# Kernel optimization log

Hardware: AMD Instinct MI355X
Metric: run time of the kernel (lower is better)

The kernel has to match this reference:

```python
import jax, jax.numpy as jnp
import numpy as np

B, S, D, H = 8, 1024, 1024, 16
DH = D // H
LN_EPS = 1e-5
SLOPE = 0.01  # nn.LeakyReLU default negative_slope


def _ln(x, g, b):
    m = x.mean(-1, keepdims=True)
    v = ((x - m) ** 2).mean(-1, keepdims=True)
    return (x - m) / jnp.sqrt(v + LN_EPS) * g + b


def _leaky(x):
    return jnp.where(x >= 0, x, SLOPE * x)


def setup_inputs() -> dict:
    key = jax.random.key(0)
    ks = jax.random.split(key, 6)
    q = jax.random.normal(ks[0], (B, S, D), dtype=jnp.float32)
    masks = jnp.ones((B, S), dtype=jnp.int32)  # all-valid mask (masked_fill is a no-op)
    w1 = jax.random.normal(ks[1], (D, D), dtype=jnp.float32) * 0.02
    b1 = jnp.zeros((D,), jnp.float32)
    w2 = jax.random.normal(ks[2], (D, D), dtype=jnp.float32) * 0.02
    b2 = jnp.zeros((D,), jnp.float32)
    ones = jnp.ones((D,), jnp.float32)
    zeros = jnp.zeros((D,), jnp.float32)
    return dict(q=q, masks=masks,
                w1=w1, b1=b1, ln1_g=ones, ln1_b=zeros,
                w2=w2, b2=b2, ln2_g=ones, ln2_b=zeros,
                anf_g=ones, anf_b=zeros,
                an1_g=ones, an1_b=zeros,
                an2_g=ones, an2_b=zeros)


def reference(q, masks, w1, b1, ln1_g, ln1_b, w2, b2, ln2_g, ln2_b,
              anf_g, anf_b, an1_g, an1_b, an2_g, an2_b):
    # --- multi-head cosine-similarity attention (k = v = q, no projections) ---
    qh = q.reshape(B, S, H, DH).transpose(0, 2, 1, 3)  # (B,H,S,DH) == separate_heads
    qn = qh / jnp.clip(jnp.linalg.norm(qh, axis=-1, keepdims=True), 1e-8)
    # cosine similarity scores, softmax over keys
    w = jax.nn.softmax(jnp.einsum('bhqd,bhkd->bhqk', qn, qn), axis=-1)
    # masked_fill AFTER softmax (faithful to source: mask per (batch, query))
    w = jnp.where(masks[:, None, :, None] == 0, jnp.float32(-1e9), w)
    heads = jnp.einsum('bhqk,bhkd->bhqd', w, qh)
    attn = heads.transpose(0, 2, 1, 3).reshape(B, S, D)  # concat_heads
    # --- add_norm1 (dropout=0.5 but eval mode => identity) ---
    y1 = _ln(q + attn, an1_g, an1_b)
    # --- PositionWiseFFN: Linear->LN->LeakyReLU x2, then internal AddNorm ---
    h = _leaky(_ln(y1 @ w1 + b1, ln1_g, ln1_b))
    y = _leaky(_ln(h @ w2 + b2, ln2_g, ln2_b))
    y2 = _ln(y1 + y, anf_g, anf_b)
    # --- add_norm2 ---
    return _ln(y1 + y2, an2_g, an2_b)
```

## Files before the change

kernel.cpp:

```cpp
#include <hip/hip_runtime.h>
#include <hip/hip_bf16.h>

#define BB 8
#define SS 1024
#define DD 1024
#define HH 16

typedef __attribute__((ext_vector_type(8))) short short8;
typedef __attribute__((ext_vector_type(8))) __bf16 bf16x8;
typedef __attribute__((ext_vector_type(4))) float f32x4;

__device__ inline float bf2f(unsigned short h){
  unsigned u = ((unsigned)h) << 16;
  return __builtin_bit_cast(float, u);
}
__device__ inline unsigned short f2bf(float f){
  unsigned u = __builtin_bit_cast(unsigned, f);
  u += 0x7fffu + ((u >> 16) & 1u);
  return (unsigned short)(u >> 16);
}
__device__ inline f32x4 mfma16(short8 a, short8 b, f32x4 c){
  return __builtin_amdgcn_mfma_f32_16x16x32_bf16(
      __builtin_bit_cast(bf16x8, a), __builtin_bit_cast(bf16x8, b), c, 0, 0, 0);
}
__device__ inline void gld_lds16(const unsigned short* g, unsigned short* l){
  __builtin_amdgcn_global_load_lds((const __attribute__((address_space(1))) void*)g,
      (__attribute__((address_space(3))) void*)l, 16, 0, 0);
}

__global__ __launch_bounds__(256) void prep_w(const float* __restrict__ w1,
                                              const float* __restrict__ w2,
                                              unsigned short* __restrict__ w1T,
                                              unsigned short* __restrict__ w2T){
  __shared__ float tile[64][65];
  const float* src = blockIdx.z ? w2 : w1;
  unsigned short* dst = blockIdx.z ? w2T : w1T;
  int k0 = blockIdx.x * 64, n0 = blockIdx.y * 64;
  int tx = threadIdx.x & 63, ty = threadIdx.x >> 6;
#pragma unroll
  for (int r = 0; r < 16; ++r)
    tile[ty + 4*r][tx] = src[(k0 + ty + 4*r) * DD + n0 + tx];
  __syncthreads();
#pragma unroll
  for (int r = 0; r < 16; ++r)
    dst[(n0 + ty + 4*r) * DD + k0 + tx] = f2bf(tile[tx][ty + 4*r]);
}

__global__ __launch_bounds__(256) void prep_q(const float* __restrict__ q,
                                              unsigned short* __restrict__ kf,
                                              unsigned short* __restrict__ vf,
                                              unsigned short* __restrict__ qb){
  __shared__ float tile[64][65];
  __shared__ float rinv[64];
  int bh = blockIdx.x >> 4, st = blockIdx.x & 15;
  int b = bh >> 4, h = bh & 15;
  int t = threadIdx.x;
  int tx = t & 63, ty = t >> 6;
  int srow = b * SS + st * 64;
#pragma unroll
  for (int r = 0; r < 16; ++r)
    tile[ty + 4*r][tx] = q[(size_t)(srow + ty + 4*r) * DD + h * 64 + tx];
  __syncthreads();
  {
    int s = t >> 2, p = t & 3;
    float ssum = 0.f;
#pragma unroll
    for (int i = 0; i < 16; ++i){ float v = tile[s][p*16 + i]; ssum += v * v; }
    ssum += __shfl_xor(ssum, 1);
    ssum += __shfl_xor(ssum, 2);
    if (p == 0) rinv[s] = 1.0f / fmaxf(sqrtf(ssum), 1e-8f);
  }
  __syncthreads();
#pragma unroll
  for (int r = 0; r < 16; ++r)
    qb[(size_t)(srow + ty + 4*r) * DD + h * 64 + tx] = f2bf(tile[ty + 4*r][tx]);
#pragma unroll
  for (int v = 0; v < 2; ++v){
    int idx = t * 2 + v;
    int c_l = idx >> 6, lane = idx & 63;
    int g2 = c_l >> 2, c = (c_l >> 1) & 1, hf = c_l & 1;
    int lrq = lane & 15, lgq = lane >> 4;
    int s = g2 * 32 + (lrq >> 2) * 8 + c * 4 + (lrq & 3);
    int d0 = hf * 32 + lgq * 8;
    float rv = rinv[s] * 1.20112240878645f;
    short8 o;
#pragma unroll
    for (int e = 0; e < 8; ++e) o[e] = (short)f2bf(tile[s][d0 + e] * rv);
    *(short8*)(kf + ((size_t)(bh * 128 + st * 8 + c_l) * 64 + lane) * 8) = o;
  }
#pragma unroll
  for (int v = 0; v < 2; ++v){
    int idx = t * 2 + v;
    int kt2 = idx >> 8, db = (idx >> 6) & 3, lane = idx & 63;
    int d = db * 16 + (lane & 15);
    int k0 = kt2 * 32 + (lane >> 4) * 8;
    short8 o;
#pragma unroll
    for (int e = 0; e < 8; ++e) o[e] = (short)f2bf(tile[k0 + e][d]);
    *(short8*)(vf + ((size_t)((bh * 32 + st * 2 + kt2) * 4 + db) * 512 + lane * 8)) = o;
  }
}

#define NPH 16
__global__ __launch_bounds__(512, 4) void attn_kern(const unsigned short* __restrict__ kf,
                                                    const unsigned short* __restrict__ vf,
                                                    const int* __restrict__ masks,
                                                    unsigned short* __restrict__ attnb){
  __shared__ unsigned short Kb[3][8][512];
  __shared__ unsigned short Vb[3][8][512];
  __shared__ int anym;
  const int bh = blockIdx.x, b = bh >> 4, h = bh & 15;
  const int by = blockIdx.y;
  const int t = threadIdx.x, w = t >> 6, l = t & 63;
  const int lr = l & 15, lg = l >> 4;
  if (t == 0) anym = 0;
  __syncthreads();
  if (t < 256 && masks[b * SS + by * 256 + t] == 0) anym = 1;

  short8 aQ[2][2];
#pragma unroll
  for (int c = 0; c < 2; ++c)
#pragma unroll
    for (int hf = 0; hf < 2; ++hf)
      aQ[c][hf] = *(const short8*)(kf +
          ((size_t)(bh * 128 + (by * 8 + w) * 4 + c * 2 + hf) * 64 + l) * 8);

  const short ONEB = (short)0x3F80;
  const short8 ones = {ONEB, ONEB, ONEB, ONEB, ONEB, ONEB, ONEB, ONEB};

#define STAGE(ph, bf) do {                                                            \
    if (w < 4){                                                                       \
      gld_lds16(kf + ((size_t)(bh * 128 + (2*(ph)) * 4 + w) * 64 + l) * 8,            \
                &Kb[bf][w][0]);                                                       \
      gld_lds16(kf + ((size_t)(bh * 128 + (2*(ph)+1) * 4 + w) * 64 + l) * 8,          \
                &Kb[bf][4 + w][0]);                                                   \
    } else {                                                                          \
      gld_lds16(vf + ((size_t)((bh * 32 + 2*(ph)) * 4 + (w - 4)) * 512 + l * 8),      \
                &Vb[bf][w - 4][0]);                                                   \
      gld_lds16(vf + ((size_t)((bh * 32 + 2*(ph)+1) * 4 + (w - 4)) * 512 + l * 8),    \
                &Vb[bf][4 + (w - 4)][0]);                                             \
    }                                                                                 \
  } while (0)

  STAGE(0, 0);
  STAGE(1, 1);
  asm volatile("s_waitcnt vmcnt(2) lgkmcnt(0)" ::: "memory");
  __builtin_amdgcn_s_barrier();

  f32x4 o[2][4] = {};
  f32x4 rsacc[2] = {};

  for (int ph = 0; ph < NPH; ++ph){
    const int cur = ph % 3;
    if (ph + 2 < NPH) STAGE(ph + 2, (ph + 2) % 3);
#pragma unroll
    for (int gi = 0; gi < 2; ++gi){
      short8 bK[2][2];
#pragma unroll
      for (int c = 0; c < 2; ++c)
#pragma unroll
        for (int hf = 0; hf < 2; ++hf)
          bK[c][hf] = *(const short8*)&Kb[cur][gi * 4 + c * 2 + hf][l * 8];
      f32x4 sc[2][2];
#pragma unroll
      for (int qc = 0; qc < 2; ++qc)
#pragma unroll
        for (int c = 0; c < 2; ++c){
          f32x4 z = {0.f, 0.f, 0.f, 0.f};
          z = mfma16(bK[c][0], aQ[qc][0], z);
          z = mfma16(bK[c][1], aQ[qc][1], z);
          sc[qc][c] = z;
        }
      bf16x8 pav[2];
#pragma unroll
      for (int qc = 0; qc < 2; ++qc)
#pragma unroll
        for (int c = 0; c < 2; ++c)
#pragma unroll
          for (int j = 0; j < 4; ++j){
            float x = sc[qc][c][j], pv;
            asm("v_exp_f32 %0, %1" : "=v"(pv) : "v"(x));
            pav[qc][c * 4 + j] = (__bf16)pv;
          }
      short8 pa0 = __builtin_bit_cast(short8, pav[0]);
      short8 pa1 = __builtin_bit_cast(short8, pav[1]);
      rsacc[0] = mfma16(pa0, ones, rsacc[0]);
      rsacc[1] = mfma16(pa1, ones, rsacc[1]);
#pragma unroll
      for (int db = 0; db < 4; ++db){
        short8 bV = *(const short8*)&Vb[cur][gi * 4 + db][l * 8];
        o[0][db] = mfma16(pa0, bV, o[0][db]);
        o[1][db] = mfma16(pa1, bV, o[1][db]);
      }
    }
    if (ph + 1 < NPH){
      asm volatile("s_waitcnt lgkmcnt(0)" ::: "memory");
      if (ph + 2 < NPH) asm volatile("s_waitcnt vmcnt(2)" ::: "memory");
      else              asm volatile("s_waitcnt vmcnt(0)" ::: "memory");
      __builtin_amdgcn_s_barrier();
    }
  }

#pragma unroll
  for (int qc = 0; qc < 2; ++qc){
    float invj[4];
#pragma unroll
    for (int j = 0; j < 4; ++j) invj[j] = 1.0f / rsacc[qc][j];
#pragma unroll
    for (int db = 0; db < 4; ++db)
#pragma unroll
      for (int j = 0; j < 4; ++j){
        int qrow = by * 256 + w * 32 + lg * 8 + qc * 4 + j;
        float val = o[qc][db][j] * invj[j];
        if (anym && masks[b * SS + qrow] == 0){
          float vs = 0.f;
          for (int kt = 0; kt < 32; ++kt)
            for (int lgp = 0; lgp < 4; ++lgp){
              const unsigned short* vp = vf +
                  ((size_t)((bh * 32 + kt) * 4 + db) * 512 + (lgp * 16 + lr) * 8);
              for (int e = 0; e < 8; ++e) vs += bf2f(vp[e]);
            }
          val = -1e9f * vs;
        }
        attnb[(size_t)(b * SS + qrow) * DD + h * 64 + db * 16 + lr] = f2bf(val);
      }
  }
#undef STAGE
}

__device__ inline float2 br2(float a, float bq){
  __shared__ float sm[8];
#pragma unroll
  for (int off = 1; off < 64; off <<= 1){
    a += __shfl_xor(a, off);
    bq += __shfl_xor(bq, off);
  }
  int w = threadIdx.x >> 6;
  if ((threadIdx.x & 63) == 0){ sm[w * 2] = a; sm[w * 2 + 1] = bq; }
  __syncthreads();
  int base = (threadIdx.x >> 7) * 4;
  float2 r;
  r.x = sm[base] + sm[base + 2];
  r.y = sm[base + 1] + sm[base + 3];
  __syncthreads();
  return r;
}

__global__ __launch_bounds__(256) void addnorm1(const unsigned short* __restrict__ qb,
                                                const unsigned short* __restrict__ attnb,
                                                const float* __restrict__ g,
                                                const float* __restrict__ bt,
                                                unsigned short* __restrict__ y1b){
  int rg = threadIdx.x >> 7, tt = threadIdx.x & 127;
  int row = blockIdx.x * 2 + rg;
  short8 qv = *(const short8*)(qb + (size_t)row * DD + tt * 8);
  short8 av = *(const short8*)(attnb + (size_t)row * DD + tt * 8);
  float x[8]; float s = 0.f, ssq = 0.f;
#pragma unroll
  for (int i = 0; i < 8; ++i){
    x[i] = bf2f((unsigned short)qv[i]) + bf2f((unsigned short)av[i]);
    s += x[i]; ssq += x[i] * x[i];
  }
  float2 r = br2(s, ssq);
  float m = r.x * (1.0f / DD);
  float rs = rsqrtf(r.y * (1.0f / DD) - m * m + 1e-5f);
  float4 g0 = *(const float4*)(g + tt * 8), g1 = *(const float4*)(g + tt * 8 + 4);
  float4 b0 = *(const float4*)(bt + tt * 8), b1 = *(const float4*)(bt + tt * 8 + 4);
  float gg[8] = {g0.x,g0.y,g0.z,g0.w,g1.x,g1.y,g1.z,g1.w};
  float bb[8] = {b0.x,b0.y,b0.z,b0.w,b1.x,b1.y,b1.z,b1.w};
  short8 ob;
#pragma unroll
  for (int i = 0; i < 8; ++i) ob[i] = (short)f2bf((x[i]-m)*rs*gg[i] + bb[i]);
  *(short8*)(y1b + (size_t)row * DD + tt * 8) = ob;
}

__global__ __launch_bounds__(256, 2) void gemm_bias(const unsigned short* __restrict__ X,
                                                    const unsigned short* __restrict__ WT,
                                                    const float* __restrict__ bias,
                                                    unsigned short* __restrict__ out){
  __shared__ unsigned short LDSB[24576];
  int t = threadIdx.x, l = t & 63, w = t >> 6;
  int wm = w >> 1, wn = w & 1;
  int lr = l & 15, lg = l >> 4;
  int bm = blockIdx.x * 128, bn = blockIdx.y * 128;
  f32x4 acc[4][4] = {};
  int r = t >> 2, cb = (t & 3) * 8;

#define ASP(bf) (LDSB + (bf) * 4096)
#define BSP(bf) (LDSB + 12288 + (bf) * 4096)
#define GSTAGE(kt, bf) do {                                                        \
    gld_lds16(X  + (size_t)(bm +      r) * 1024 + (kt) * 32 + cb,                  \
              ASP(bf) + w * 512);                                                  \
    gld_lds16(X  + (size_t)(bm + 64 + r) * 1024 + (kt) * 32 + cb,                  \
              ASP(bf) + 2048 + w * 512);                                           \
    gld_lds16(WT + (size_t)(bn +      r) * 1024 + (kt) * 32 + cb,                  \
              BSP(bf) + w * 512);                                                  \
    gld_lds16(WT + (size_t)(bn + 64 + r) * 1024 + (kt) * 32 + cb,                  \
              BSP(bf) + 2048 + w * 512);                                           \
  } while (0)

  GSTAGE(0, 0);
  GSTAGE(1, 1);
  asm volatile("s_waitcnt vmcnt(4)" ::: "memory");
  __builtin_amdgcn_s_barrier();

  for (int kt = 0; kt < 32; ++kt){
    const int cur = kt % 3;
    if (kt + 2 < 32) GSTAGE(kt + 2, (kt + 2) % 3);
    short8 aA[4], bB[4];
#pragma unroll
    for (int i = 0; i < 4; ++i)
      aA[i] = *(const short8*)(ASP(cur) + (wm * 64 + i * 16 + lr) * 32 + lg * 8);
#pragma unroll
    for (int i = 0; i < 4; ++i)
      bB[i] = *(const short8*)(BSP(cur) + (wn * 64 + i * 16 + lr) * 32 + lg * 8);
    __builtin_amdgcn_s_setprio(1);
#pragma unroll
    for (int mi = 0; mi < 4; ++mi)
#pragma unroll
      for (int ni = 0; ni < 4; ++ni)
        acc[mi][ni] = mfma16(aA[mi], bB[ni], acc[mi][ni]);
    __builtin_amdgcn_s_setprio(0);
    if (kt + 1 < 32){
      asm volatile("s_waitcnt lgkmcnt(0)" ::: "memory");
      if (kt + 2 < 32) asm volatile("s_waitcnt vmcnt(4)" ::: "memory");
      else             asm volatile("s_waitcnt vmcnt(0)" ::: "memory");
      __builtin_amdgcn_s_barrier();
    }
  }
#undef GSTAGE

  asm volatile("s_waitcnt lgkmcnt(0)" ::: "memory");
  __builtin_amdgcn_s_barrier();
#pragma unroll
  for (int ni = 0; ni < 4; ++ni){
    int col = wn * 64 + ni * 16 + lr;
    float bv = bias[bn + col];
#pragma unroll
    for (int mi = 0; mi < 4; ++mi){
      int row0 = wm * 64 + mi * 16 + lg * 4;
#pragma unroll
      for (int j = 0; j < 4; ++j)
        LDSB[(row0 + j) * 128 + col] = f2bf(acc[mi][ni][j] + bv);
    }
  }
  asm volatile("s_waitcnt lgkmcnt(0)" ::: "memory");
  __builtin_amdgcn_s_barrier();
#pragma unroll
  for (int i = 0; i < 8; ++i){
    int idx = t + i * 256;
    int row = idx >> 4;
    int c8  = idx & 15;
    short8 v = *(const short8*)&LDSB[row * 128 + c8 * 8];
    *(short8*)(out + (size_t)(bm + row) * 1024 + bn + c8 * 8) = v;
  }
#undef ASP
#undef BSP
}

__global__ __launch_bounds__(256) void ln_leaky(const unsigned short* __restrict__ in,
                                                const float* __restrict__ g,
                                                const float* __restrict__ bt,
                                                unsigned short* __restrict__ out){
  int rg = threadIdx.x >> 7, tt = threadIdx.x & 127;
  int row = blockIdx.x * 2 + rg;
  short8 iv = *(const short8*)(in + (size_t)row * DD + tt * 8);
  float x[8]; float s = 0.f, ssq = 0.f;
#pragma unroll
  for (int i = 0; i < 8; ++i){
    x[i] = bf2f((unsigned short)iv[i]);
    s += x[i]; ssq += x[i] * x[i];
  }
  float2 r = br2(s, ssq);
  float m = r.x * (1.0f / DD);
  float rs = rsqrtf(r.y * (1.0f / DD) - m * m + 1e-5f);
  float4 g0 = *(const float4*)(g + tt * 8), g1 = *(const float4*)(g + tt * 8 + 4);
  float4 b0 = *(const float4*)(bt + tt * 8), b1 = *(const float4*)(bt + tt * 8 + 4);
  float gg[8] = {g0.x,g0.y,g0.z,g0.w,g1.x,g1.y,g1.z,g1.w};
  float bb[8] = {b0.x,b0.y,b0.z,b0.w,b1.x,b1.y,b1.z,b1.w};
  short8 ov;
#pragma unroll
  for (int i = 0; i < 8; ++i){
    float v = (x[i]-m)*rs*gg[i] + bb[i];
    v = v >= 0.f ? v : 0.01f * v;
    ov[i] = (short)f2bf(v);
  }
  *(short8*)(out + (size_t)row * DD + tt * 8) = ov;
}

__global__ __launch_bounds__(256) void final_kern(const unsigned short* __restrict__ g2,
                                                  const unsigned short* __restrict__ y1,
                                                  const float* __restrict__ ln2g, const float* __restrict__ ln2b,
                                                  const float* __restrict__ anfg, const float* __restrict__ anfb,
                                                  const float* __restrict__ an2g, const float* __restrict__ an2b,
                                                  float* __restrict__ out){
  int rg = threadIdx.x >> 7, tt = threadIdx.x & 127;
  int row = blockIdx.x * 2 + rg;
  short8 iv = *(const short8*)(g2 + (size_t)row * DD + tt * 8);
  short8 yv = *(const short8*)(y1 + (size_t)row * DD + tt * 8);
  float x[8], yy1[8]; float s = 0.f, ssq = 0.f;
#pragma unroll
  for (int i = 0; i < 8; ++i){
    x[i] = bf2f((unsigned short)iv[i]);
    yy1[i] = bf2f((unsigned short)yv[i]);
    s += x[i]; ssq += x[i] * x[i];
  }
  float2 r = br2(s, ssq);
  float m = r.x * (1.0f / DD);
  float rs = rsqrtf(r.y * (1.0f / DD) - m * m + 1e-5f);
  float4 p0, p1;
  p0 = *(const float4*)(ln2g + tt * 8); p1 = *(const float4*)(ln2g + tt * 8 + 4);
  float gg[8] = {p0.x,p0.y,p0.z,p0.w,p1.x,p1.y,p1.z,p1.w};
  p0 = *(const float4*)(ln2b + tt * 8); p1 = *(const float4*)(ln2b + tt * 8 + 4);
  float bb[8] = {p0.x,p0.y,p0.z,p0.w,p1.x,p1.y,p1.z,p1.w};
  float y[8];
#pragma unroll
  for (int i = 0; i < 8; ++i){
    float v = (x[i]-m)*rs*gg[i] + bb[i];
    y[i] = v >= 0.f ? v : 0.01f * v;
  }

  float tv[8]; s = 0.f; ssq = 0.f;
#pragma unroll
  for (int i = 0; i < 8; ++i){ tv[i] = yy1[i] + y[i]; s += tv[i]; ssq += tv[i]*tv[i]; }
  r = br2(s, ssq);
  m = r.x * (1.0f / DD);
  rs = rsqrtf(r.y * (1.0f / DD) - m*m + 1e-5f);
  p0 = *(const float4*)(anfg + tt * 8); p1 = *(const float4*)(anfg + tt * 8 + 4);
  float gg2[8] = {p0.x,p0.y,p0.z,p0.w,p1.x,p1.y,p1.z,p1.w};
  p0 = *(const float4*)(anfb + tt * 8); p1 = *(const float4*)(anfb + tt * 8 + 4);
  float bb2[8] = {p0.x,p0.y,p0.z,p0.w,p1.x,p1.y,p1.z,p1.w};
  float y2[8];
#pragma unroll
  for (int i = 0; i < 8; ++i) y2[i] = (tv[i]-m)*rs*gg2[i] + bb2[i];

  float u[8]; s = 0.f; ssq = 0.f;
#pragma unroll
  for (int i = 0; i < 8; ++i){ u[i] = yy1[i] + y2[i]; s += u[i]; ssq += u[i]*u[i]; }
  r = br2(s, ssq);
  m = r.x * (1.0f / DD);
  rs = rsqrtf(r.y * (1.0f / DD) - m*m + 1e-5f);
  p0 = *(const float4*)(an2g + tt * 8); p1 = *(const float4*)(an2g + tt * 8 + 4);
  float gg3[8] = {p0.x,p0.y,p0.z,p0.w,p1.x,p1.y,p1.z,p1.w};
  p0 = *(const float4*)(an2b + tt * 8); p1 = *(const float4*)(an2b + tt * 8 + 4);
  float bb3[8] = {p0.x,p0.y,p0.z,p0.w,p1.x,p1.y,p1.z,p1.w};
  float4 o0 = { (u[0]-m)*rs*gg3[0] + bb3[0], (u[1]-m)*rs*gg3[1] + bb3[1],
                (u[2]-m)*rs*gg3[2] + bb3[2], (u[3]-m)*rs*gg3[3] + bb3[3] };
  float4 o1 = { (u[4]-m)*rs*gg3[4] + bb3[4], (u[5]-m)*rs*gg3[5] + bb3[5],
                (u[6]-m)*rs*gg3[6] + bb3[6], (u[7]-m)*rs*gg3[7] + bb3[7] };
  *(float4*)(out + (size_t)row * DD + tt * 8) = o0;
  *(float4*)(out + (size_t)row * DD + tt * 8 + 4) = o1;
}

extern "C" void kernel_launch(void* const* d_in, const int* in_sizes, int n_in,
                              void* d_out, int out_size, void* d_ws, size_t ws_size,
                              hipStream_t stream){
  const float* q    = (const float*)d_in[0];
  const int* masks  = (const int*)d_in[1];
  const float* w1   = (const float*)d_in[2];
  const float* b1   = (const float*)d_in[3];
  const float* ln1g = (const float*)d_in[4];
  const float* ln1b = (const float*)d_in[5];
  const float* w2   = (const float*)d_in[6];
  const float* b2   = (const float*)d_in[7];
  const float* ln2g = (const float*)d_in[8];
  const float* ln2b = (const float*)d_in[9];
  const float* anfg = (const float*)d_in[10];
  const float* anfb = (const float*)d_in[11];
  const float* an1g = (const float*)d_in[12];
  const float* an1b = (const float*)d_in[13];
  const float* an2g = (const float*)d_in[14];
  const float* an2b = (const float*)d_in[15];

  char* ws = (char*)d_ws;
  unsigned short* w1T  = (unsigned short*)(ws + 0);
  unsigned short* w2T  = (unsigned short*)(ws + 2097152);
  unsigned short* kf   = (unsigned short*)(ws + 4194304);
  unsigned short* vf   = (unsigned short*)(ws + 20971520);
  unsigned short* attn = (unsigned short*)(ws + 37748736);
  unsigned short* y1b  = (unsigned short*)(ws + 54525952);
  unsigned short* qb   = (unsigned short*)(ws + 71303168);
  unsigned short* g1   = kf;
  unsigned short* hbuf = vf;
  unsigned short* g2   = attn;
  float* outp = (float*)d_out;

  prep_w<<<dim3(16, 16, 2), 256, 0, stream>>>(w1, w2, w1T, w2T);
  prep_q<<<dim3(2048), 256, 0, stream>>>(q, kf, vf, qb);
  attn_kern<<<dim3(128, 4), 512, 0, stream>>>(kf, vf, masks, attn);
  addnorm1<<<dim3(4096), 256, 0, stream>>>(qb, attn, an1g, an1b, y1b);
  gemm_bias<<<dim3(64, 8), 256, 0, stream>>>(y1b, w1T, b1, g1);
  ln_leaky<<<dim3(4096), 256, 0, stream>>>(g1, ln1g, ln1b, hbuf);
  gemm_bias<<<dim3(64, 8), 256, 0, stream>>>(hbuf, w2T, b2, g2);
  final_kern<<<dim3(4096), 256, 0, stream>>>(g2, y1b, ln2g, ln2b, anfg, anfb, an2g, an2b, outp);
}
```

Baseline: 144.1 us.

## Halve attention block to 4 waves, each computing 64 query rows

The attention kernel now runs 256 threads per block instead of 512. Each wave handles four 16-row query chunks instead of two, so every K/V fragment read from LDS feeds twice as many MFMAs. Staging is redistributed so each of the four waves issues four global-to-LDS loads per phase, and the vmcnt waits are adjusted to match. This cuts LDS read traffic and barrier participants per unit of work. In exchange it raises register pressure (larger accumulators, launch bounds lowered) and gives fewer waves per CU to hide latency.

Result: no change. 142.5 us (-1.2%).

```diff
diff --git a/kernel.cpp b/kernel.cpp
--- a/kernel.cpp
+++ b/kernel.cpp
@@ -102,7 +102,7 @@
 }
 
 #define NPH 16
-__global__ __launch_bounds__(512, 4) void attn_kern(const unsigned short* __restrict__ kf,
+__global__ __launch_bounds__(256, 2) void attn_kern(const unsigned short* __restrict__ kf,
                                                     const unsigned short* __restrict__ vf,
                                                     const int* __restrict__ masks,
                                                     unsigned short* __restrict__ attnb){
@@ -115,40 +115,40 @@
   const int lr = l & 15, lg = l >> 4;
   if (t == 0) anym = 0;
   __syncthreads();
-  if (t < 256 && masks[b * SS + by * 256 + t] == 0) anym = 1;
-
-  short8 aQ[2][2];
-#pragma unroll
-  for (int c = 0; c < 2; ++c)
+  if (masks[b * SS + by * 256 + t] == 0) anym = 1;
+
+  short8 aQ[4][2];
+#pragma unroll
+  for (int qc = 0; qc < 4; ++qc)
 #pragma unroll
     for (int hf = 0; hf < 2; ++hf)
-      aQ[c][hf] = *(const short8*)(kf +
-          ((size_t)(bh * 128 + (by * 8 + w) * 4 + c * 2 + hf) * 64 + l) * 8);
+      aQ[qc][hf] = *(const short8*)(kf +
+          ((size_t)(bh * 128 + (by * 8 + w * 2 + (qc >> 1)) * 4 + (qc & 1) * 2 + hf) * 64 + l) * 8);
 
   const short ONEB = (short)0x3F80;
   const short8 ones = {ONEB, ONEB, ONEB, ONEB, ONEB, ONEB, ONEB, ONEB};
 
 #define STAGE(ph, bf) do {                                                            \
-    if (w < 4){                                                                       \
-      gld_lds16(kf + ((size_t)(bh * 128 + (2*(ph)) * 4 + w) * 64 + l) * 8,            \
-                &Kb[bf][w][0]);                                                       \
-      gld_lds16(kf + ((size_t)(bh * 128 + (2*(ph)+1) * 4 + w) * 64 + l) * 8,          \
-                &Kb[bf][4 + w][0]);                                                   \
+    if (w < 2){                                                                       \
+      _Pragma("unroll")                                                               \
+      for (int i = 0; i < 4; ++i)                                                     \
+        gld_lds16(kf + ((size_t)(bh * 128 + (2*(ph) + w) * 4 + i) * 64 + l) * 8,      \
+                  &Kb[bf][w * 4 + i][0]);                                             \
     } else {                                                                          \
-      gld_lds16(vf + ((size_t)((bh * 32 + 2*(ph)) * 4 + (w - 4)) * 512 + l * 8),      \
-                &Vb[bf][w - 4][0]);                                                   \
-      gld_lds16(vf + ((size_t)((bh * 32 + 2*(ph)+1) * 4 + (w - 4)) * 512 + l * 8),    \
-                &Vb[bf][4 + (w - 4)][0]);                                             \
+      _Pragma("unroll")                                                               \
+      for (int i = 0; i < 4; ++i)                                                     \
+        gld_lds16(vf + ((size_t)((bh * 32 + 2*(ph) + (w - 2)) * 4 + i) * 512 + l * 8),\
+                  &Vb[bf][(w - 2) * 4 + i][0]);                                       \
     }                                                                                 \
   } while (0)
 
   STAGE(0, 0);
   STAGE(1, 1);
-  asm volatile("s_waitcnt vmcnt(2) lgkmcnt(0)" ::: "memory");
+  asm volatile("s_waitcnt vmcnt(4) lgkmcnt(0)" ::: "memory");
   __builtin_amdgcn_s_barrier();
 
-  f32x4 o[2][4] = {};
-  f32x4 rsacc[2] = {};
+  f32x4 o[4][4] = {};
+  f32x4 rsacc[4] = {};
 
   for (int ph = 0; ph < NPH; ++ph){
     const int cur = ph % 3;
@@ -161,9 +161,9 @@
 #pragma unroll
         for (int hf = 0; hf < 2; ++hf)
           bK[c][hf] = *(const short8*)&Kb[cur][gi * 4 + c * 2 + hf][l * 8];
-      f32x4 sc[2][2];
-#pragma unroll
-      for (int qc = 0; qc < 2; ++qc)
+      f32x4 sc[4][2];
+#pragma unroll
+      for (int qc = 0; qc < 4; ++qc)
 #pragma unroll
         for (int c = 0; c < 2; ++c){
           f32x4 z = {0.f, 0.f, 0.f, 0.f};
@@ -171,38 +171,41 @@
           z = mfma16(bK[c][1], aQ[qc][1], z);
           sc[qc][c] = z;
         }
-      bf16x8 pav[2];
-#pragma unroll
-      for (int qc = 0; qc < 2; ++qc)
+      short8 pa[4];
+#pragma unroll
+      for (int qc = 0; qc < 4; ++qc){
+        bf16x8 pav;
 #pragma unroll
         for (int c = 0; c < 2; ++c)
 #pragma unroll
           for (int j = 0; j < 4; ++j){
             float x = sc[qc][c][j], pv;
             asm("v_exp_f32 %0, %1" : "=v"(pv) : "v"(x));
-            pav[qc][c * 4 + j] = (__bf16)pv;
+            pav[c * 4 + j] = (__bf16)pv;
           }
-      short8 pa0 = __builtin_bit_cast(short8, pav[0]);
-      short8 pa1 = __builtin_bit_cast(short8, pav[1]);
-      rsacc[0] = mfma16(pa0, ones, rsacc[0]);
-      rsacc[1] = mfma16(pa1, ones, rsacc[1]);
+        pa[qc] = __builtin_bit_cast(short8, pav);
+      }
+#pragma unroll
+      for (int qc = 0; qc < 4; ++qc)
+        rsacc[qc] = mfma16(pa[qc], ones, rsacc[qc]);
 #pragma unroll
       for (int db = 0; db < 4; ++db){
         short8 bV = *(const short8*)&Vb[cur][gi * 4 + db][l * 8];
-        o[0][db] = mfma16(pa0, bV, o[0][db]);
-        o[1][db] = mfma16(pa1, bV, o[1][db]);
+#pragma unroll
+        for (int qc = 0; qc < 4; ++qc)
+          o[qc][db] = mfma16(pa[qc], bV, o[qc][db]);
       }
     }
     if (ph + 1 < NPH){
       asm volatile("s_waitcnt lgkmcnt(0)" ::: "memory");
-      if (ph + 2 < NPH) asm volatile("s_waitcnt vmcnt(2)" ::: "memory");
+      if (ph + 2 < NPH) asm volatile("s_waitcnt vmcnt(4)" ::: "memory");
       else              asm volatile("s_waitcnt vmcnt(0)" ::: "memory");
       __builtin_amdgcn_s_barrier();
     }
   }
 
 #pragma unroll
-  for (int qc = 0; qc < 2; ++qc){
+  for (int qc = 0; qc < 4; ++qc){
     float invj[4];
 #pragma unroll
     for (int j = 0; j < 4; ++j) invj[j] = 1.0f / rsacc[qc][j];
@@ -210,7 +213,7 @@
     for (int db = 0; db < 4; ++db)
 #pragma unroll
       for (int j = 0; j < 4; ++j){
-        int qrow = by * 256 + w * 32 + lg * 8 + qc * 4 + j;
+        int qrow = by * 256 + (w * 2 + (qc >> 1)) * 32 + lg * 8 + (qc & 1) * 4 + j;
         float val = o[qc][db][j] * invj[j];
         if (anym && masks[b * SS + qrow] == 0){
           float vs = 0.f;
@@ -487,7 +490,7 @@
 
   prep_w<<<dim3(16, 16, 2), 256, 0, stream>>>(w1, w2, w1T, w2T);
   prep_q<<<dim3(2048), 256, 0, stream>>>(q, kf, vf, qb);
-  attn_kern<<<dim3(128, 4), 512, 0, stream>>>(kf, vf, masks, attn);
+  attn_kern<<<dim3(128, 4), 256, 0, stream>>>(kf, vf, masks, attn);
   addnorm1<<<dim3(4096), 256, 0, stream>>>(qb, attn, an1g, an1b, y1b);
   gemm_bias<<<dim3(64, 8), 256, 0, stream>>>(y1b, w1T, b1, g1);
   ln_leaky<<<dim3(4096), 256, 0, stream>>>(g1, ln1g, ln1b, hbuf);
```
